# Kernel tuning notes

Hardware: AMD Instinct MI355X
Metric: run time of the kernel (lower is better)

Reference implementation:

```python
import jax, jax.numpy as jnp
import numpy as np

INPUT_SIZE = 128
HIDDEN_SIZE = 128
BATCH = 65536


def _xavier(key, shape):
    fan_out, fan_in = shape
    limit = np.sqrt(6.0 / (fan_in + fan_out)).astype(np.float32)
    return jax.random.uniform(key, shape, jnp.float32, -limit, limit)


def setup_inputs() -> dict:
    key = jax.random.key(0)
    ks = jax.random.split(key, 12)
    inp = {
        "x": jax.random.normal(ks[0], (BATCH, INPUT_SIZE), jnp.float32),
        "h_t": jax.random.normal(ks[1], (BATCH, HIDDEN_SIZE), jnp.float32),
        "c_t": jax.random.normal(ks[2], (BATCH, HIDDEN_SIZE), jnp.float32),
        "W_ii": _xavier(ks[3], (HIDDEN_SIZE, INPUT_SIZE)),
        "W_hi": _xavier(ks[4], (HIDDEN_SIZE, HIDDEN_SIZE)),
        "b_i": jnp.zeros((HIDDEN_SIZE,), jnp.float32),
        "W_if": _xavier(ks[5], (HIDDEN_SIZE, INPUT_SIZE)),
        "W_hf": _xavier(ks[6], (HIDDEN_SIZE, HIDDEN_SIZE)),
        "b_f": jnp.zeros((HIDDEN_SIZE,), jnp.float32),
        "W_ig": _xavier(ks[7], (HIDDEN_SIZE, INPUT_SIZE)),
        "W_hg": _xavier(ks[8], (HIDDEN_SIZE, HIDDEN_SIZE)),
        "b_g": jnp.zeros((HIDDEN_SIZE,), jnp.float32),
        "W_io": _xavier(ks[9], (HIDDEN_SIZE, INPUT_SIZE)),
        "W_ho": _xavier(ks[10], (HIDDEN_SIZE, HIDDEN_SIZE)),
        "b_o": jnp.zeros((HIDDEN_SIZE,), jnp.float32),
    }
    return inp


def reference(x, h_t, c_t, W_ii, W_hi, b_i, W_if, W_hf, b_f, W_ig, W_hg, b_g, W_io, W_ho, b_o):
    # Fuse the 8 small GEMMs into 2 concatenated GEMMs, identical math to
    # per-gate F.linear calls (same weights, just stacked along output dim).
    W_x = jnp.concatenate([W_ii, W_if, W_ig, W_io], axis=0)   # [4H, I]
    W_h = jnp.concatenate([W_hi, W_hf, W_hg, W_ho], axis=0)   # [4H, H]
    b = jnp.concatenate([b_i, b_f, b_g, b_o], axis=0)         # [4H]
    gates = x @ W_x.T + h_t @ W_h.T + b                       # [B, 4H]
    i_a, f_a, g_a, o_a = jnp.split(gates, 4, axis=1)
    i_t = jax.nn.sigmoid(i_a)
    f_t = jax.nn.sigmoid(f_a)
    g_t = jnp.tanh(g_a)
    o_t = jax.nn.sigmoid(o_a)
    c_new = f_t * c_t + i_t * g_t
    h_new = o_t * jnp.tanh(c_new)
    return (h_new, c_new)
```

## Files before the change

kernel.cpp:

```cpp
#include <hip/hip_runtime.h>
#include <hip/hip_bf16.h>


typedef short s16x8 __attribute__((ext_vector_type(8)));
typedef float f32x4 __attribute__((ext_vector_type(4)));

__device__ __forceinline__ short f2bf(float f) {
    __hip_bfloat16 h = __float2bfloat16(f);
    return __builtin_bit_cast(short, h);
}
__device__ __forceinline__ float sigm(float x) { return 1.0f / (1.0f + __expf(-x)); }
__device__ __forceinline__ float tanh_f(float x) { return 1.0f - 2.0f / (1.0f + __expf(2.0f * x)); }

__global__ __launch_bounds__(256, 2)
void lstm_cell_kernel(const float* __restrict__ X,
                      const float* __restrict__ H,
                      const float* __restrict__ C,
                      const float* __restrict__ Wii, const float* __restrict__ Whi, const float* __restrict__ Bi,
                      const float* __restrict__ Wif, const float* __restrict__ Whf, const float* __restrict__ Bf,
                      const float* __restrict__ Wig, const float* __restrict__ Whg, const float* __restrict__ Bg,
                      const float* __restrict__ Wio, const float* __restrict__ Who, const float* __restrict__ Bo,
                      float* __restrict__ OutH,
                      float* __restrict__ OutC)
{
    __shared__ short sA[128 * 128];
    __shared__ short sB[128 * 128];

    const int tid = threadIdx.x;
    const int l  = tid & 63;
    const int w  = tid >> 6;
    const int wm = w & 1;
    const int wn = w >> 1;
    const int lj = l & 15;
    const int lq = l >> 4;

    const int jt = blockIdx.x & 3;
    const int bb = blockIdx.x >> 2;
    const int B0 = bb * 128;
    const int J0 = jt * 32;

    f32x4 acc[4][4];
#pragma unroll
    for (int mt = 0; mt < 4; ++mt)
#pragma unroll
        for (int g = 0; g < 4; ++g)
            acc[mt][g] = (f32x4){0.f, 0.f, 0.f, 0.f};

#pragma unroll
    for (int half = 0; half < 2; ++half) {
        const float* Asrc = half ? H : X;

#pragma unroll
        for (int tt = 0; tt < 2; ++tt) {
            f32x4 f[4][2];
#pragma unroll
            for (int t = 0; t < 4; ++t) {
                const int cc   = (tt * 4 + t) * 256 + tid;
                const int m    = cc >> 4;
                const int oct  = cc & 15;
                const int soct = oct ^ (m & 15);
                const float* src = Asrc + (size_t)(B0 + m) * 128 + soct * 8;
                f[t][0] = *(const f32x4*)src;
                f[t][1] = *(const f32x4*)(src + 4);
            }
#pragma unroll
            for (int t = 0; t < 4; ++t) {
                const int cc = (tt * 4 + t) * 256 + tid;
                s16x8 v;
#pragma unroll
                for (int k = 0; k < 4; ++k) {
                    v[k]     = f2bf(f[t][0][k]);
                    v[4 + k] = f2bf(f[t][1][k]);
                }
                *(s16x8*)(sA + cc * 8) = v;
            }
        }
#pragma unroll
        for (int tt = 0; tt < 2; ++tt) {
            f32x4 f[4][2];
#pragma unroll
            for (int t = 0; t < 4; ++t) {
                const int cc   = (tt * 4 + t) * 256 + tid;
                const int cl   = cc >> 4;
                const int oct  = cc & 15;
                const int soct = oct ^ (cl & 15);
                const int gate = (cl >> 4) & 3;
                const int j    = J0 + ((cl >> 6) << 4) + (cl & 15);
                const float* wp;
                if (half == 0)
                    wp = (gate == 0) ? Wii : (gate == 1) ? Wif : (gate == 2) ? Wig : Wio;
                else
                    wp = (gate == 0) ? Whi : (gate == 1) ? Whf : (gate == 2) ? Whg : Who;
                const float* src = wp + (size_t)j * 128 + soct * 8;
                f[t][0] = *(const f32x4*)src;
                f[t][1] = *(const f32x4*)(src + 4);
            }
#pragma unroll
            for (int t = 0; t < 4; ++t) {
                const int cc = (tt * 4 + t) * 256 + tid;
                s16x8 v;
#pragma unroll
                for (int k = 0; k < 4; ++k) {
                    v[k]     = f2bf(f[t][0][k]);
                    v[4 + k] = f2bf(f[t][1][k]);
                }
                *(s16x8*)(sB + cc * 8) = v;
            }
        }
        __syncthreads();

#pragma unroll
        for (int ks = 0; ks < 4; ++ks) {
            const int oct = (ks * 4 + lq) ^ lj;
            s16x8 af[4], bf[4];
#pragma unroll
            for (int mt = 0; mt < 4; ++mt) {
                const int m = wm * 64 + mt * 16 + lj;
                af[mt] = *(const s16x8*)(sA + m * 128 + oct * 8);
            }
#pragma unroll
            for (int g = 0; g < 4; ++g) {
                const int cl = wn * 64 + g * 16 + lj;
                bf[g] = *(const s16x8*)(sB + cl * 128 + oct * 8);
            }
#pragma unroll
            for (int mt = 0; mt < 4; ++mt)
#pragma unroll
                for (int g = 0; g < 4; ++g)
                    acc[mt][g] = __builtin_amdgcn_mfma_f32_16x16x32_bf16(
                        af[mt], bf[g], acc[mt][g], 0, 0, 0);
        }
        __syncthreads();
    }

    const int j = J0 + wn * 16 + lj;
    const float bi  = Bi[j];
    const float bfv = Bf[j];
    const float bg  = Bg[j];
    const float bo  = Bo[j];

#pragma unroll
    for (int mt = 0; mt < 4; ++mt) {
#pragma unroll
        for (int r = 0; r < 4; ++r) {
            const int b   = B0 + wm * 64 + mt * 16 + lq * 4 + r;
            const size_t idx = (size_t)b * 128 + j;
            const float ia = acc[mt][0][r] + bi;
            const float fa = acc[mt][1][r] + bfv;
            const float ga = acc[mt][2][r] + bg;
            const float oa = acc[mt][3][r] + bo;
            const float it = sigm(ia);
            const float ft = sigm(fa);
            const float gt = tanh_f(ga);
            const float ot = sigm(oa);
            const float co = C[idx];
            const float cn = ft * co + it * gt;
            const float hn = ot * tanh_f(cn);
            OutH[idx] = hn;
            OutC[idx] = cn;
        }
    }
}

extern "C" void kernel_launch(void* const* d_in, const int* in_sizes, int n_in,
                              void* d_out, int out_size, void* d_ws, size_t ws_size,
                              hipStream_t stream) {
    const float* X   = (const float*)d_in[0];
    const float* H   = (const float*)d_in[1];
    const float* C   = (const float*)d_in[2];
    const float* Wii = (const float*)d_in[3];
    const float* Whi = (const float*)d_in[4];
    const float* Bi  = (const float*)d_in[5];
    const float* Wif = (const float*)d_in[6];
    const float* Whf = (const float*)d_in[7];
    const float* Bf  = (const float*)d_in[8];
    const float* Wig = (const float*)d_in[9];
    const float* Whg = (const float*)d_in[10];
    const float* Bg  = (const float*)d_in[11];
    const float* Wio = (const float*)d_in[12];
    const float* Who = (const float*)d_in[13];
    const float* Bo  = (const float*)d_in[14];

    float* OutH = (float*)d_out;
    float* OutC = OutH + (size_t)65536 * 128;

    dim3 grid(2048), block(256);
    hipLaunchKernelGGL(lstm_cell_kernel, grid, block, 0, stream,
                       X, H, C, Wii, Whi, Bi, Wif, Whf, Bf,
                       Wig, Whg, Bg, Wio, Who, Bo, OutH, OutC);
}
```

Before: 205.6 us.

## Pre-pack bf16 weights in MFMA fragment order and load B directly into registers

Adds a small pre-kernel that converts the eight weight matrices to bf16 once per call and stores them in workspace, laid out in the per-lane MFMA fragment order. The main kernel then loads B fragments straight from global memory into registers, which removes the sB shared buffer, its fp32-to-bf16 conversion and its LDS reads. With half the LDS in use, the occupancy hint rises to 3 blocks per CU. The costs are an extra kernel launch, a larger live register set for the 16 held B fragments, and global reads of the packed weights that now depend on cache hits.

```diff
diff --git a/kernel.cpp b/kernel.cpp
--- a/kernel.cpp
+++ b/kernel.cpp
@@ -12,19 +12,48 @@
 __device__ __forceinline__ float sigm(float x) { return 1.0f / (1.0f + __expf(-x)); }
 __device__ __forceinline__ float tanh_f(float x) { return 1.0f - 2.0f / (1.0f + __expf(2.0f * x)); }
 
-__global__ __launch_bounds__(256, 2)
+__global__ __launch_bounds__(256)
+void repack_weights(const float* __restrict__ Wii, const float* __restrict__ Whi,
+                    const float* __restrict__ Wif, const float* __restrict__ Whf,
+                    const float* __restrict__ Wig, const float* __restrict__ Whg,
+                    const float* __restrict__ Wio, const float* __restrict__ Who,
+                    short* __restrict__ ws)
+{
+    const int t     = blockIdx.x * 256 + threadIdx.x;
+    const int chunk = t >> 6;
+    const int l     = t & 63;
+    const int ks    = chunk & 3;
+    const int half  = (chunk >> 2) & 1;
+    const int g     = (chunk >> 3) & 3;
+    const int wn    = (chunk >> 5) & 1;
+    const int jt    = chunk >> 6;
+    const int j     = jt * 32 + wn * 16 + (l & 15);
+    const int k0    = (ks * 4 + (l >> 4)) * 8;
+
+    const float* wp;
+    if (half == 0) wp = (g == 0) ? Wii : (g == 1) ? Wif : (g == 2) ? Wig : Wio;
+    else           wp = (g == 0) ? Whi : (g == 1) ? Whf : (g == 2) ? Whg : Who;
+
+    const float* src = wp + (size_t)j * 128 + k0;
+    f32x4 a = *(const f32x4*)src;
+    f32x4 b = *(const f32x4*)(src + 4);
+    s16x8 v;
+#pragma unroll
+    for (int k = 0; k < 4; ++k) { v[k] = f2bf(a[k]); v[4 + k] = f2bf(b[k]); }
+    *(s16x8*)(ws + (size_t)t * 8) = v;
+}
+
+__global__ __launch_bounds__(256, 3)
 void lstm_cell_kernel(const float* __restrict__ X,
                       const float* __restrict__ H,
                       const float* __restrict__ C,
-                      const float* __restrict__ Wii, const float* __restrict__ Whi, const float* __restrict__ Bi,
-                      const float* __restrict__ Wif, const float* __restrict__ Whf, const float* __restrict__ Bf,
-                      const float* __restrict__ Wig, const float* __restrict__ Whg, const float* __restrict__ Bg,
-                      const float* __restrict__ Wio, const float* __restrict__ Who, const float* __restrict__ Bo,
+                      const float* __restrict__ Bi, const float* __restrict__ Bf,
+                      const float* __restrict__ Bg, const float* __restrict__ Bo,
+                      const short* __restrict__ WS,
                       float* __restrict__ OutH,
                       float* __restrict__ OutC)
 {
     __shared__ short sA[128 * 128];
-    __shared__ short sB[128 * 128];
 
     const int tid = threadIdx.x;
     const int l  = tid & 63;
@@ -46,9 +75,18 @@
         for (int g = 0; g < 4; ++g)
             acc[mt][g] = (f32x4){0.f, 0.f, 0.f, 0.f};
 
+    const short* wsbase = WS + ((size_t)(jt * 2 + wn) * 32) * 512 + l * 8;
+
 #pragma unroll
     for (int half = 0; half < 2; ++half) {
         const float* Asrc = half ? H : X;
+
+        s16x8 bfh[4][4];
+#pragma unroll
+        for (int g = 0; g < 4; ++g)
+#pragma unroll
+            for (int ks = 0; ks < 4; ++ks)
+                bfh[g][ks] = *(const s16x8*)(wsbase + (size_t)((g * 2 + half) * 4 + ks) * 512);
 
 #pragma unroll
         for (int tt = 0; tt < 2; ++tt) {
@@ -75,60 +113,23 @@
                 *(s16x8*)(sA + cc * 8) = v;
             }
         }
-#pragma unroll
-        for (int tt = 0; tt < 2; ++tt) {
-            f32x4 f[4][2];
-#pragma unroll
-            for (int t = 0; t < 4; ++t) {
-                const int cc   = (tt * 4 + t) * 256 + tid;
-                const int cl   = cc >> 4;
-                const int oct  = cc & 15;
-                const int soct = oct ^ (cl & 15);
-                const int gate = (cl >> 4) & 3;
-                const int j    = J0 + ((cl >> 6) << 4) + (cl & 15);
-                const float* wp;
-                if (half == 0)
-                    wp = (gate == 0) ? Wii : (gate == 1) ? Wif : (gate == 2) ? Wig : Wio;
-                else
-                    wp = (gate == 0) ? Whi : (gate == 1) ? Whf : (gate == 2) ? Whg : Who;
-                const float* src = wp + (size_t)j * 128 + soct * 8;
-                f[t][0] = *(const f32x4*)src;
-                f[t][1] = *(const f32x4*)(src + 4);
-            }
-#pragma unroll
-            for (int t = 0; t < 4; ++t) {
-                const int cc = (tt * 4 + t) * 256 + tid;
-                s16x8 v;
-#pragma unroll
-                for (int k = 0; k < 4; ++k) {
-                    v[k]     = f2bf(f[t][0][k]);
-                    v[4 + k] = f2bf(f[t][1][k]);
-                }
-                *(s16x8*)(sB + cc * 8) = v;
-            }
-        }
         __syncthreads();
 
 #pragma unroll
         for (int ks = 0; ks < 4; ++ks) {
             const int oct = (ks * 4 + lq) ^ lj;
-            s16x8 af[4], bf[4];
+            s16x8 af[4];
 #pragma unroll
             for (int mt = 0; mt < 4; ++mt) {
                 const int m = wm * 64 + mt * 16 + lj;
                 af[mt] = *(const s16x8*)(sA + m * 128 + oct * 8);
             }
 #pragma unroll
-            for (int g = 0; g < 4; ++g) {
-                const int cl = wn * 64 + g * 16 + lj;
-                bf[g] = *(const s16x8*)(sB + cl * 128 + oct * 8);
-            }
-#pragma unroll
             for (int mt = 0; mt < 4; ++mt)
 #pragma unroll
                 for (int g = 0; g < 4; ++g)
                     acc[mt][g] = __builtin_amdgcn_mfma_f32_16x16x32_bf16(
-                        af[mt], bf[g], acc[mt][g], 0, 0, 0);
+                        af[mt], bfh[g][ks], acc[mt][g], 0, 0, 0);
         }
         __syncthreads();
     }
@@ -181,11 +182,14 @@
     const float* Who = (const float*)d_in[13];
     const float* Bo  = (const float*)d_in[14];
 
+    short* ws = (short*)d_ws;
+
+    hipLaunchKernelGGL(repack_weights, dim3(64), dim3(256), 0, stream,
+                       Wii, Whi, Wif, Whf, Wig, Whg, Wio, Who, ws);
+
     float* OutH = (float*)d_out;
     float* OutC = OutH + (size_t)65536 * 128;
 
-    dim3 grid(2048), block(256);
-    hipLaunchKernelGGL(lstm_cell_kernel, grid, block, 0, stream,
-                       X, H, C, Wii, Whi, Bi, Wif, Whf, Bf,
-                       Wig, Whg, Bg, Wio, Who, Bo, OutH, OutC);
+    hipLaunchKernelGGL(lstm_cell_kernel, dim3(2048), dim3(256), 0, stream,
+                       X, H, C, Bi, Bf, Bg, Bo, ws, OutH, OutC);
 }
```

Result: faster. 197.7 us (-3.9%).
